# Kernel optimization log

Measured on AMD Instinct MI355X. Metric: run time of the kernel, lower is better.

The kernel has to match this reference:

```python
import jax, jax.numpy as jnp
import numpy as np

N_NODES = 50000
N_EDGES = 300000
IN_FEATS = 128
N_HIDDEN = 64
N_HEADS = 4
N_CLASSES = 47
NEG_SLOPE = 0.2


def setup_inputs() -> dict:
    key = jax.random.key(0)
    ks = jax.random.split(key, 16)
    s = 0.1
    inp = {
        "x": jax.random.normal(ks[0], (N_NODES, IN_FEATS), jnp.float32),
        "src": jax.random.randint(ks[1], (N_EDGES,), 0, N_NODES, jnp.int64 if jax.config.jax_enable_x64 else jnp.int32),
        "dst": jax.random.randint(ks[2], (N_EDGES,), 0, N_NODES, jnp.int64 if jax.config.jax_enable_x64 else jnp.int32),
        # layer 1: in_feats -> (heads, hidden)
        "W1": jax.random.normal(ks[3], (IN_FEATS, N_HEADS * N_HIDDEN), jnp.float32) * s,
        "al1": jax.random.normal(ks[4], (N_HEADS, N_HIDDEN), jnp.float32) * s,
        "ar1": jax.random.normal(ks[5], (N_HEADS, N_HIDDEN), jnp.float32) * s,
        "b1": jnp.zeros((N_HEADS * N_HIDDEN,), jnp.float32),
        # layer 2: heads*hidden -> (heads, hidden)
        "W2": jax.random.normal(ks[6], (N_HEADS * N_HIDDEN, N_HEADS * N_HIDDEN), jnp.float32) * s,
        "al2": jax.random.normal(ks[7], (N_HEADS, N_HIDDEN), jnp.float32) * s,
        "ar2": jax.random.normal(ks[8], (N_HEADS, N_HIDDEN), jnp.float32) * s,
        "b2": jnp.zeros((N_HEADS * N_HIDDEN,), jnp.float32),
        # layer 3: heads*hidden -> (1, n_classes)
        "W3": jax.random.normal(ks[9], (N_HEADS * N_HIDDEN, N_CLASSES), jnp.float32) * s,
        "al3": jax.random.normal(ks[10], (1, N_CLASSES), jnp.float32) * s,
        "ar3": jax.random.normal(ks[11], (1, N_CLASSES), jnp.float32) * s,
        "b3": jnp.zeros((N_CLASSES,), jnp.float32),
    }
    return inp


def gat_conv(h, src, dst, W, al, ar, b, n_nodes):
    """DGL GATConv (shared src/dst projection, edge-softmax over dst)."""
    H, D = al.shape
    feat = (h @ W).reshape(n_nodes, H, D)              # [N,H,D]
    el = jnp.sum(feat * al[None], axis=-1)             # [N,H]
    er = jnp.sum(feat * ar[None], axis=-1)             # [N,H]
    e = jax.nn.leaky_relu(el[src] + er[dst], NEG_SLOPE)  # [E,H]
    emax = jax.ops.segment_max(e, dst, num_segments=n_nodes)  # [N,H]
    emax = jnp.where(jnp.isfinite(emax), emax, 0.0)    # empty segments
    ee = jnp.exp(e - emax[dst])                        # [E,H]
    denom = jax.ops.segment_sum(ee, dst, num_segments=n_nodes)  # [N,H]
    alpha = ee / jnp.maximum(denom[dst], 1e-9)         # [E,H]
    msg = feat[src] * alpha[..., None]                 # [E,H,D]
    out = jax.ops.segment_sum(msg, dst, num_segments=n_nodes)   # [N,H,D]
    return out + b.reshape(1, H, D)


def reference(x, src, dst, W1, al1, ar1, b1, W2, al2, ar2, b2, W3, al3, ar3, b3):
    n = x.shape[0]
    h = gat_conv(x, src, dst, W1, al1, ar1, b1, n).reshape(n, -1)  # flatten heads
    h = gat_conv(h, src, dst, W2, al2, ar2, b2, n).reshape(n, -1)
    h = gat_conv(h, src, dst, W3, al3, ar3, b3, n)                 # [N,1,C]
    return h.mean(axis=1)                                          # [N,C]
```

## Files before the change

### kernel.cpp

```cpp
#include <hip/hip_runtime.h>
#include <cstddef>

#define GAT_N 50000
#define GAT_E 300000
#define SCAN_B 256

typedef short bf16x8 __attribute__((ext_vector_type(8)));
typedef float f32x4  __attribute__((ext_vector_type(4)));

__device__ __forceinline__ ushort f2bf(float f) {
    unsigned u = __float_as_uint(f);
    return (ushort)((u + 0x7fffu + ((u >> 16) & 1u)) >> 16);
}
__device__ __forceinline__ float bf2f(ushort h) {
    return __uint_as_float((unsigned)h << 16);
}


__global__ __launch_bounds__(256) void zero_ints(int* __restrict__ a, int n) {
    int i = blockIdx.x * blockDim.x + threadIdx.x;
    int stride = gridDim.x * blockDim.x;
    for (; i < n; i += stride) a[i] = 0;
}

__global__ __launch_bounds__(256) void count_k(
    const int* __restrict__ dst, int* __restrict__ cnt, int E)
{
    int e = blockIdx.x * blockDim.x + threadIdx.x;
    if (e < E) atomicAdd(&cnt[dst[e]], 1);
}

__global__ __launch_bounds__(256) void csr_partial(
    const int* __restrict__ cnt, int* __restrict__ partials, int N, int chunk)
{
    __shared__ int red[256];
    int b = blockIdx.x, t = threadIdx.x;
    int s = 0;
    for (int i = t; i < chunk; i += 256) {
        int idx = b * chunk + i;
        if (idx < N) s += cnt[idx];
    }
    red[t] = s;
    __syncthreads();
    for (int off = 128; off > 0; off >>= 1) {
        if (t < off) red[t] += red[t + off];
        __syncthreads();
    }
    if (t == 0) partials[b] = red[0];
}

__global__ __launch_bounds__(SCAN_B) void csr_scanp(
    int* __restrict__ partials, int* __restrict__ rowptr, int N)
{
    __shared__ int sc[SCAN_B];
    int t = threadIdx.x;
    int v = partials[t];
    sc[t] = v;
    __syncthreads();
    for (int off = 1; off < SCAN_B; off <<= 1) {
        int u = (t >= off) ? sc[t - off] : 0;
        __syncthreads();
        sc[t] += u;
        __syncthreads();
    }
    partials[t] = sc[t] - v;
    if (t == SCAN_B - 1) rowptr[N] = sc[t];
}

__global__ __launch_bounds__(256) void csr_write(
    const int* __restrict__ cnt, const int* __restrict__ partials,
    int* __restrict__ rowptr, int N, int chunk)
{
    __shared__ int sc[256];
    int b = blockIdx.x, t = threadIdx.x;
    int idx = b * chunk + t;
    int v = (t < chunk && idx < N) ? cnt[idx] : 0;
    sc[t] = v;
    __syncthreads();
    for (int off = 1; off < 256; off <<= 1) {
        int u = (t >= off) ? sc[t - off] : 0;
        __syncthreads();
        sc[t] += u;
        __syncthreads();
    }
    if (t < chunk && idx < N) rowptr[idx] = partials[b] + sc[t] - v;
}

__global__ __launch_bounds__(256) void scatter_k(
    const int* __restrict__ src, const int* __restrict__ dst,
    const int* __restrict__ rowptr, int* __restrict__ cursor,
    int* __restrict__ ssrc, int* __restrict__ sdst, int E)
{
    int e = blockIdx.x * blockDim.x + threadIdx.x;
    if (e >= E) return;
    int d = dst[e];
    int p = rowptr[d] + atomicAdd(&cursor[d], 1);
    ssrc[p] = src[e];
    sdst[p] = d;
}


__global__ __launch_bounds__(256) void convert_x(
    const float* __restrict__ x, ushort* __restrict__ Xh, ushort* __restrict__ Xl,
    long total4)
{
    long i = (long)blockIdx.x * blockDim.x + threadIdx.x;
    long stride = (long)gridDim.x * blockDim.x;
    for (; i < total4; i += stride) {
        float4 v = *(const float4*)(x + i * 4);
        ushort4 h, lo;
        h.x = f2bf(v.x); lo.x = f2bf(v.x - bf2f(h.x));
        h.y = f2bf(v.y); lo.y = f2bf(v.y - bf2f(h.y));
        h.z = f2bf(v.z); lo.z = f2bf(v.z - bf2f(h.z));
        h.w = f2bf(v.w); lo.w = f2bf(v.w - bf2f(h.w));
        *(ushort4*)(Xh + i * 4) = h;
        *(ushort4*)(Xl + i * 4) = lo;
    }
}

__global__ __launch_bounds__(256) void convert_w(
    const float* __restrict__ W, ushort* __restrict__ Wth, ushort* __restrict__ Wtl,
    int K, int M, int Mp)
{
    int idx = blockIdx.x * blockDim.x + threadIdx.x;
    if (idx >= Mp * K) return;
    int c = idx / K, k = idx - c * K;
    float v = (c < M) ? W[(size_t)k * M + c] : 0.f;
    ushort h = f2bf(v);
    Wth[idx] = h;
    Wtl[idx] = f2bf(v - bf2f(h));
}


#define LDK 40

__global__ __launch_bounds__(256) void gemm_feat(
    const ushort* __restrict__ Ah, const ushort* __restrict__ Al,
    const ushort* __restrict__ Wh, const ushort* __restrict__ Wl,
    const float* __restrict__ alw, const float* __restrict__ arw,
    float* __restrict__ feat, float* __restrict__ el, float* __restrict__ er,
    int N, int K, int M, int H, int D, int ldF)
{
    __shared__ ushort As_h[128 * LDK];
    __shared__ ushort As_l[128 * LDK];
    __shared__ ushort Bs_h[128 * LDK];
    __shared__ ushort Bs_l[128 * LDK];

    const int m0 = blockIdx.x * 128;
    const int n0 = blockIdx.y * 128;
    const int t = threadIdx.x;
    const int w = t >> 6, lane = t & 63;
    const int lr = lane & 15, lg = lane >> 4;
    const int wr = (w >> 1) * 64, wc = (w & 1) * 64;

    f32x4 acc[4][4] = {};

    for (int k0 = 0; k0 < K; k0 += 32) {
        #pragma unroll
        for (int l = 0; l < 2; ++l) {
            int idx = t + l * 256;
            int row = idx >> 2, kk = (idx & 3) * 8;
            bf16x8 vh = {}, vl = {};
            int gr = m0 + row;
            if (gr < N) {
                vh = *(const bf16x8*)(Ah + (size_t)gr * K + k0 + kk);
                vl = *(const bf16x8*)(Al + (size_t)gr * K + k0 + kk);
            }
            bf16x8 wh = *(const bf16x8*)(Wh + (size_t)(n0 + row) * K + k0 + kk);
            bf16x8 wl = *(const bf16x8*)(Wl + (size_t)(n0 + row) * K + k0 + kk);
            *(bf16x8*)&As_h[row * LDK + kk] = vh;
            *(bf16x8*)&As_l[row * LDK + kk] = vl;
            *(bf16x8*)&Bs_h[row * LDK + kk] = wh;
            *(bf16x8*)&Bs_l[row * LDK + kk] = wl;
        }
        __syncthreads();

        bf16x8 a_h[4], a_l[4];
        #pragma unroll
        for (int fi = 0; fi < 4; ++fi) {
            a_h[fi] = *(const bf16x8*)&As_h[(wr + fi * 16 + lr) * LDK + lg * 8];
            a_l[fi] = *(const bf16x8*)&As_l[(wr + fi * 16 + lr) * LDK + lg * 8];
        }
        #pragma unroll
        for (int fj = 0; fj < 4; ++fj) {
            bf16x8 b_h = *(const bf16x8*)&Bs_h[(wc + fj * 16 + lr) * LDK + lg * 8];
            bf16x8 b_l = *(const bf16x8*)&Bs_l[(wc + fj * 16 + lr) * LDK + lg * 8];
            #pragma unroll
            for (int fi = 0; fi < 4; ++fi) {
                acc[fi][fj] = __builtin_amdgcn_mfma_f32_16x16x32_bf16(a_h[fi], b_h, acc[fi][fj], 0, 0, 0);
                acc[fi][fj] = __builtin_amdgcn_mfma_f32_16x16x32_bf16(a_l[fi], b_h, acc[fi][fj], 0, 0, 0);
                acc[fi][fj] = __builtin_amdgcn_mfma_f32_16x16x32_bf16(a_h[fi], b_l, acc[fi][fj], 0, 0, 0);
            }
        }
        __syncthreads();
    }

    #pragma unroll
    for (int fi = 0; fi < 4; ++fi) {
        #pragma unroll
        for (int q = 0; q < 4; ++q) {
            int row = m0 + wr + fi * 16 + 4 * lg + q;
            if (row < N) {
                #pragma unroll
                for (int fj = 0; fj < 4; ++fj) {
                    int col = n0 + wc + fj * 16 + lr;
                    if (col < M) feat[(size_t)row * ldF + col] = acc[fi][fj][q];
                }
            }
        }
    }

    const int head = (n0 + wc) / D;
    if (head < H) {
        float alv[4], arv[4];
        #pragma unroll
        for (int fj = 0; fj < 4; ++fj) {
            int col = n0 + wc + fj * 16 + lr;
            alv[fj] = (col < M) ? alw[col] : 0.f;
            arv[fj] = (col < M) ? arw[col] : 0.f;
        }
        #pragma unroll
        for (int fi = 0; fi < 4; ++fi) {
            #pragma unroll
            for (int q = 0; q < 4; ++q) {
                float s1 = 0.f, s2 = 0.f;
                #pragma unroll
                for (int fj = 0; fj < 4; ++fj) {
                    s1 = fmaf(acc[fi][fj][q], alv[fj], s1);
                    s2 = fmaf(acc[fi][fj][q], arv[fj], s2);
                }
                #pragma unroll
                for (int mask = 1; mask <= 8; mask <<= 1) {
                    s1 += __shfl_xor(s1, mask);
                    s2 += __shfl_xor(s2, mask);
                }
                int row = m0 + wr + fi * 16 + 4 * lg + q;
                if (lr == 0 && row < N) {
                    el[(size_t)row * H + head] = s1;
                    er[(size_t)row * H + head] = s2;
                }
            }
        }
    }
}


__global__ __launch_bounds__(256) void edge_score4(
    const int* __restrict__ ssrc, const int* __restrict__ sdst,
    const float* __restrict__ el, const float* __restrict__ er,
    float* __restrict__ sc, int E)
{
    int p = blockIdx.x * blockDim.x + threadIdx.x;
    if (p >= E) return;
    int s = ssrc[p], d = sdst[p];
    float4 a = *(const float4*)(el + (size_t)s * 4);
    float4 b = *(const float4*)(er + (size_t)d * 4);
    float4 v;
    v.x = a.x + b.x; v.x = v.x > 0.f ? v.x : 0.2f * v.x;
    v.y = a.y + b.y; v.y = v.y > 0.f ? v.y : 0.2f * v.y;
    v.z = a.z + b.z; v.z = v.z > 0.f ? v.z : 0.2f * v.z;
    v.w = a.w + b.w; v.w = v.w > 0.f ? v.w : 0.2f * v.w;
    *(float4*)(sc + (size_t)p * 4) = v;
}

__global__ __launch_bounds__(256) void edge_score1(
    const int* __restrict__ ssrc, const int* __restrict__ sdst,
    const float* __restrict__ el, const float* __restrict__ er,
    float* __restrict__ sc, int E)
{
    int p = blockIdx.x * blockDim.x + threadIdx.x;
    if (p >= E) return;
    float v = el[ssrc[p]] + er[sdst[p]];
    sc[p] = v > 0.f ? v : 0.2f * v;
}


__global__ __launch_bounds__(256) void node_aggr256(
    const int* __restrict__ rowptr, const int* __restrict__ ssrc,
    const float* __restrict__ sc, const float* __restrict__ feat,
    const float* __restrict__ bias,
    ushort* __restrict__ Ah_out, ushort* __restrict__ Al_out, int N)
{
    int n = blockIdx.x * 4 + (threadIdx.x >> 6);
    if (n >= N) return;
    int lane = threadIdx.x & 63;
    int h = lane >> 4, sub = lane & 15;
    int beg = rowptr[n], end = rowptr[n + 1];

    float m = -__builtin_inff();
    for (int j = beg + sub; j < end; j += 16)
        m = fmaxf(m, sc[(size_t)j * 4 + h]);
    #pragma unroll
    for (int mask = 1; mask <= 8; mask <<= 1)
        m = fmaxf(m, __shfl_xor(m, mask));

    float denom = 0.f;
    for (int j = beg + sub; j < end; j += 16)
        denom += __expf(sc[(size_t)j * 4 + h] - m);
    #pragma unroll
    for (int mask = 1; mask <= 8; mask <<= 1)
        denom += __shfl_xor(denom, mask);

    float inv = 1.f / fmaxf(denom, 1e-9f);
    float ax = 0.f, ay = 0.f, az = 0.f, aw = 0.f;
    for (int j = beg; j < end; ++j) {
        float wgt = __expf(sc[(size_t)j * 4 + h] - m);
        int s = ssrc[j];
        float4 f = *(const float4*)(feat + (size_t)s * 256 + lane * 4);
        ax = fmaf(wgt, f.x, ax);
        ay = fmaf(wgt, f.y, ay);
        az = fmaf(wgt, f.z, az);
        aw = fmaf(wgt, f.w, aw);
    }
    float v0 = fmaf(ax, inv, bias[lane * 4 + 0]);
    float v1 = fmaf(ay, inv, bias[lane * 4 + 1]);
    float v2 = fmaf(az, inv, bias[lane * 4 + 2]);
    float v3 = fmaf(aw, inv, bias[lane * 4 + 3]);
    ushort4 hh, lo;
    hh.x = f2bf(v0); lo.x = f2bf(v0 - bf2f(hh.x));
    hh.y = f2bf(v1); lo.y = f2bf(v1 - bf2f(hh.y));
    hh.z = f2bf(v2); lo.z = f2bf(v2 - bf2f(hh.z));
    hh.w = f2bf(v3); lo.w = f2bf(v3 - bf2f(hh.w));
    *(ushort4*)(Ah_out + (size_t)n * 256 + lane * 4) = hh;
    *(ushort4*)(Al_out + (size_t)n * 256 + lane * 4) = lo;
}

__global__ __launch_bounds__(256) void node_aggr47(
    const int* __restrict__ rowptr, const int* __restrict__ ssrc,
    const float* __restrict__ sc, const float* __restrict__ feat,
    const float* __restrict__ bias, float* __restrict__ out, int N)
{
    int n = blockIdx.x * 4 + (threadIdx.x >> 6);
    if (n >= N) return;
    int lane = threadIdx.x & 63;
    int beg = rowptr[n], end = rowptr[n + 1];

    float m = -__builtin_inff();
    for (int j = beg + lane; j < end; j += 64)
        m = fmaxf(m, sc[j]);
    #pragma unroll
    for (int mask = 1; mask <= 32; mask <<= 1)
        m = fmaxf(m, __shfl_xor(m, mask));

    float denom = 0.f;
    for (int j = beg + lane; j < end; j += 64)
        denom += __expf(sc[j] - m);
    #pragma unroll
    for (int mask = 1; mask <= 32; mask <<= 1)
        denom += __shfl_xor(denom, mask);

    float inv = 1.f / fmaxf(denom, 1e-9f);
    float acc = 0.f;
    for (int j = beg; j < end; ++j) {
        float wgt = __expf(sc[j] - m);
        int s = ssrc[j];
        float f = (lane < 47) ? feat[(size_t)s * 48 + lane] : 0.f;
        acc = fmaf(wgt, f, acc);
    }
    if (lane < 47)
        out[(size_t)n * 47 + lane] = fmaf(acc, inv, bias[lane]);
}


extern "C" void kernel_launch(void* const* d_in, const int* in_sizes, int n_in,
                              void* d_out, int out_size, void* d_ws, size_t ws_size,
                              hipStream_t stream) {
    const float* x   = (const float*)d_in[0];
    const int*   src = (const int*)d_in[1];
    const int*   dst = (const int*)d_in[2];
    const float* W1  = (const float*)d_in[3];
    const float* al1 = (const float*)d_in[4];
    const float* ar1 = (const float*)d_in[5];
    const float* b1  = (const float*)d_in[6];
    const float* W2  = (const float*)d_in[7];
    const float* al2 = (const float*)d_in[8];
    const float* ar2 = (const float*)d_in[9];
    const float* b2  = (const float*)d_in[10];
    const float* W3  = (const float*)d_in[11];
    const float* al3 = (const float*)d_in[12];
    const float* ar3 = (const float*)d_in[13];
    const float* b3  = (const float*)d_in[14];
    float* out = (float*)d_out;

    const int N = GAT_N, E = GAT_E;
    const int chunk = (N + SCAN_B - 1) / SCAN_B;

    char* wsb = (char*)d_ws;
    size_t o = 0;
    float*  feat  = (float*)(wsb + o);  o += (size_t)N * 256 * 4;
    ushort* Ah    = (ushort*)(wsb + o); o += (size_t)N * 256 * 2;
    ushort* Al    = (ushort*)(wsb + o); o += (size_t)N * 256 * 2;
    float*  el    = (float*)(wsb + o);  o += (size_t)N * 4 * 4;
    float*  er    = (float*)(wsb + o);  o += (size_t)N * 4 * 4;
    int* rowptr   = (int*)(wsb + o);    o += (size_t)(N + 1) * 4;
    int* cnt      = (int*)(wsb + o);    o += (size_t)N * 4;
    int* cursor   = (int*)(wsb + o);    o += (size_t)N * 4;
    int* ssrc     = (int*)(wsb + o);    o += (size_t)E * 4;
    int* sdst     = (int*)(wsb + o);    o += (size_t)E * 4;
    float* scbuf  = (float*)(wsb + o);  o += (size_t)E * 4 * 4;
    int* partials = (int*)(wsb + o);    o += (size_t)SCAN_B * 4;
    ushort* Wt1h  = (ushort*)(wsb + o); o += (size_t)256 * 128 * 2;
    ushort* Wt1l  = (ushort*)(wsb + o); o += (size_t)256 * 128 * 2;
    ushort* Wt2h  = (ushort*)(wsb + o); o += (size_t)256 * 256 * 2;
    ushort* Wt2l  = (ushort*)(wsb + o); o += (size_t)256 * 256 * 2;
    ushort* Wt3h  = (ushort*)(wsb + o); o += (size_t)128 * 256 * 2;
    ushort* Wt3l  = (ushort*)(wsb + o); o += (size_t)128 * 256 * 2;
    ushort* Xh = Ah;
    ushort* Xl = Al;

    dim3 blk(256);
    int gE = (E + 255) / 256;
    int gN = (N + 3) / 4;
    dim3 gemmG((N + 127) / 128, 2);
    dim3 gemmG3((N + 127) / 128, 1);

    zero_ints<<<64, blk, 0, stream>>>(cnt, 2 * N);
    count_k<<<gE, blk, 0, stream>>>(dst, cnt, E);
    csr_partial<<<SCAN_B, blk, 0, stream>>>(cnt, partials, N, chunk);
    csr_scanp<<<1, SCAN_B, 0, stream>>>(partials, rowptr, N);
    csr_write<<<SCAN_B, blk, 0, stream>>>(cnt, partials, rowptr, N, chunk);
    scatter_k<<<gE, blk, 0, stream>>>(src, dst, rowptr, cursor, ssrc, sdst, E);

    convert_x<<<2048, blk, 0, stream>>>(x, Xh, Xl, (long)N * 128 / 4);
    convert_w<<<(256 * 128 + 255) / 256, blk, 0, stream>>>(W1, Wt1h, Wt1l, 128, 256, 256);
    convert_w<<<(256 * 256 + 255) / 256, blk, 0, stream>>>(W2, Wt2h, Wt2l, 256, 256, 256);
    convert_w<<<(128 * 256 + 255) / 256, blk, 0, stream>>>(W3, Wt3h, Wt3l, 256, 47, 128);

    gemm_feat<<<gemmG, blk, 0, stream>>>(Xh, Xl, Wt1h, Wt1l, al1, ar1,
                                         feat, el, er, N, 128, 256, 4, 64, 256);
    edge_score4<<<gE, blk, 0, stream>>>(ssrc, sdst, el, er, scbuf, E);
    node_aggr256<<<gN, blk, 0, stream>>>(rowptr, ssrc, scbuf, feat, b1, Ah, Al, N);

    gemm_feat<<<gemmG, blk, 0, stream>>>(Ah, Al, Wt2h, Wt2l, al2, ar2,
                                         feat, el, er, N, 256, 256, 4, 64, 256);
    edge_score4<<<gE, blk, 0, stream>>>(ssrc, sdst, el, er, scbuf, E);
    node_aggr256<<<gN, blk, 0, stream>>>(rowptr, ssrc, scbuf, feat, b2, Ah, Al, N);

    gemm_feat<<<gemmG3, blk, 0, stream>>>(Ah, Al, Wt3h, Wt3l, al3, ar3,
                                          feat, el, er, N, 256, 47, 1, 47, 48);
    edge_score1<<<gE, blk, 0, stream>>>(ssrc, sdst, el, er, scbuf, E);
    node_aggr47<<<gN, blk, 0, stream>>>(rowptr, ssrc, scbuf, feat, b3, out, N);
}
```

Measured before the change: 332.2 us.

## Halve GEMM row tile to 64 and unroll edge gather loops by four

The feature GEMM now uses a 64-row tile instead of 128, doubling the grid and halving accumulator registers per thread, to raise occupancy and spread 50k rows across more blocks. Separately, the aggregation kernels for the 256-wide and 47-class layers unroll the per-edge gather loop by four so several independent feature loads are in flight at once. The smaller tile cuts reuse of the W tile, so each block reloads B more often relative to its useful work.

```diff
diff --git a/kernel.cpp b/kernel.cpp
--- a/kernel.cpp
+++ b/kernel.cpp
@@ -141,43 +141,44 @@
     float* __restrict__ feat, float* __restrict__ el, float* __restrict__ er,
     int N, int K, int M, int H, int D, int ldF)
 {
-    __shared__ ushort As_h[128 * LDK];
-    __shared__ ushort As_l[128 * LDK];
+    __shared__ ushort As_h[64 * LDK];
+    __shared__ ushort As_l[64 * LDK];
     __shared__ ushort Bs_h[128 * LDK];
     __shared__ ushort Bs_l[128 * LDK];
 
-    const int m0 = blockIdx.x * 128;
+    const int m0 = blockIdx.x * 64;
     const int n0 = blockIdx.y * 128;
     const int t = threadIdx.x;
     const int w = t >> 6, lane = t & 63;
     const int lr = lane & 15, lg = lane >> 4;
-    const int wr = (w >> 1) * 64, wc = (w & 1) * 64;
-
-    f32x4 acc[4][4] = {};
+    const int wr = (w >> 1) * 32, wc = (w & 1) * 64;
+
+    f32x4 acc[2][4] = {};
 
     for (int k0 = 0; k0 < K; k0 += 32) {
-        #pragma unroll
-        for (int l = 0; l < 2; ++l) {
-            int idx = t + l * 256;
-            int row = idx >> 2, kk = (idx & 3) * 8;
+        {
+            int row = t >> 2, kk = (t & 3) * 8;
             bf16x8 vh = {}, vl = {};
             int gr = m0 + row;
             if (gr < N) {
                 vh = *(const bf16x8*)(Ah + (size_t)gr * K + k0 + kk);
                 vl = *(const bf16x8*)(Al + (size_t)gr * K + k0 + kk);
             }
-            bf16x8 wh = *(const bf16x8*)(Wh + (size_t)(n0 + row) * K + k0 + kk);
-            bf16x8 wl = *(const bf16x8*)(Wl + (size_t)(n0 + row) * K + k0 + kk);
             *(bf16x8*)&As_h[row * LDK + kk] = vh;
             *(bf16x8*)&As_l[row * LDK + kk] = vl;
-            *(bf16x8*)&Bs_h[row * LDK + kk] = wh;
-            *(bf16x8*)&Bs_l[row * LDK + kk] = wl;
-        }
-        __syncthreads();
-
-        bf16x8 a_h[4], a_l[4];
-        #pragma unroll
-        for (int fi = 0; fi < 4; ++fi) {
+        }
+        #pragma unroll
+        for (int l = 0; l < 2; ++l) {
+            int idx = t + l * 256;
+            int row = idx >> 2, kk = (idx & 3) * 8;
+            *(bf16x8*)&Bs_h[row * LDK + kk] = *(const bf16x8*)(Wh + (size_t)(n0 + row) * K + k0 + kk);
+            *(bf16x8*)&Bs_l[row * LDK + kk] = *(const bf16x8*)(Wl + (size_t)(n0 + row) * K + k0 + kk);
+        }
+        __syncthreads();
+
+        bf16x8 a_h[2], a_l[2];
+        #pragma unroll
+        for (int fi = 0; fi < 2; ++fi) {
             a_h[fi] = *(const bf16x8*)&As_h[(wr + fi * 16 + lr) * LDK + lg * 8];
             a_l[fi] = *(const bf16x8*)&As_l[(wr + fi * 16 + lr) * LDK + lg * 8];
         }
@@ -186,7 +187,7 @@
             bf16x8 b_h = *(const bf16x8*)&Bs_h[(wc + fj * 16 + lr) * LDK + lg * 8];
             bf16x8 b_l = *(const bf16x8*)&Bs_l[(wc + fj * 16 + lr) * LDK + lg * 8];
             #pragma unroll
-            for (int fi = 0; fi < 4; ++fi) {
+            for (int fi = 0; fi < 2; ++fi) {
                 acc[fi][fj] = __builtin_amdgcn_mfma_f32_16x16x32_bf16(a_h[fi], b_h, acc[fi][fj], 0, 0, 0);
                 acc[fi][fj] = __builtin_amdgcn_mfma_f32_16x16x32_bf16(a_l[fi], b_h, acc[fi][fj], 0, 0, 0);
                 acc[fi][fj] = __builtin_amdgcn_mfma_f32_16x16x32_bf16(a_h[fi], b_l, acc[fi][fj], 0, 0, 0);
@@ -196,7 +197,7 @@
     }
 
     #pragma unroll
-    for (int fi = 0; fi < 4; ++fi) {
+    for (int fi = 0; fi < 2; ++fi) {
         #pragma unroll
         for (int q = 0; q < 4; ++q) {
             int row = m0 + wr + fi * 16 + 4 * lg + q;
@@ -220,7 +221,7 @@
             arv[fj] = (col < M) ? arw[col] : 0.f;
         }
         #pragma unroll
-        for (int fi = 0; fi < 4; ++fi) {
+        for (int fi = 0; fi < 2; ++fi) {
             #pragma unroll
             for (int q = 0; q < 4; ++q) {
                 float s1 = 0.f, s2 = 0.f;
@@ -303,7 +304,23 @@
 
     float inv = 1.f / fmaxf(denom, 1e-9f);
     float ax = 0.f, ay = 0.f, az = 0.f, aw = 0.f;
-    for (int j = beg; j < end; ++j) {
+    int j = beg;
+    for (; j + 4 <= end; j += 4) {
+        int s0 = ssrc[j + 0], s1 = ssrc[j + 1], s2 = ssrc[j + 2], s3 = ssrc[j + 3];
+        float w0 = __expf(sc[(size_t)(j + 0) * 4 + h] - m);
+        float w1 = __expf(sc[(size_t)(j + 1) * 4 + h] - m);
+        float w2 = __expf(sc[(size_t)(j + 2) * 4 + h] - m);
+        float w3 = __expf(sc[(size_t)(j + 3) * 4 + h] - m);
+        float4 f0 = *(const float4*)(feat + (size_t)s0 * 256 + lane * 4);
+        float4 f1 = *(const float4*)(feat + (size_t)s1 * 256 + lane * 4);
+        float4 f2 = *(const float4*)(feat + (size_t)s2 * 256 + lane * 4);
+        float4 f3 = *(const float4*)(feat + (size_t)s3 * 256 + lane * 4);
+        ax = fmaf(w0, f0.x, fmaf(w1, f1.x, fmaf(w2, f2.x, fmaf(w3, f3.x, ax))));
+        ay = fmaf(w0, f0.y, fmaf(w1, f1.y, fmaf(w2, f2.y, fmaf(w3, f3.y, ay))));
+        az = fmaf(w0, f0.z, fmaf(w1, f1.z, fmaf(w2, f2.z, fmaf(w3, f3.z, az))));
+        aw = fmaf(w0, f0.w, fmaf(w1, f1.w, fmaf(w2, f2.w, fmaf(w3, f3.w, aw))));
+    }
+    for (; j < end; ++j) {
         float wgt = __expf(sc[(size_t)j * 4 + h] - m);
         int s = ssrc[j];
         float4 f = *(const float4*)(feat + (size_t)s * 256 + lane * 4);
@@ -351,7 +368,20 @@
 
     float inv = 1.f / fmaxf(denom, 1e-9f);
     float acc = 0.f;
-    for (int j = beg; j < end; ++j) {
+    int j = beg;
+    for (; j + 4 <= end; j += 4) {
+        int s0 = ssrc[j + 0], s1 = ssrc[j + 1], s2 = ssrc[j + 2], s3 = ssrc[j + 3];
+        float w0 = __expf(sc[j + 0] - m);
+        float w1 = __expf(sc[j + 1] - m);
+        float w2 = __expf(sc[j + 2] - m);
+        float w3 = __expf(sc[j + 3] - m);
+        float f0 = (lane < 47) ? feat[(size_t)s0 * 48 + lane] : 0.f;
+        float f1 = (lane < 47) ? feat[(size_t)s1 * 48 + lane] : 0.f;
+        float f2 = (lane < 47) ? feat[(size_t)s2 * 48 + lane] : 0.f;
+        float f3 = (lane < 47) ? feat[(size_t)s3 * 48 + lane] : 0.f;
+        acc = fmaf(w0, f0, fmaf(w1, f1, fmaf(w2, f2, fmaf(w3, f3, acc))));
+    }
+    for (; j < end; ++j) {
         float wgt = __expf(sc[j] - m);
         int s = ssrc[j];
         float f = (lane < 47) ? feat[(size_t)s * 48 + lane] : 0.f;
@@ -411,8 +441,8 @@
     dim3 blk(256);
     int gE = (E + 255) / 256;
     int gN = (N + 3) / 4;
-    dim3 gemmG((N + 127) / 128, 2);
-    dim3 gemmG3((N + 127) / 128, 1);
+    dim3 gemmG((N + 63) / 64, 2);
+    dim3 gemmG3((N + 63) / 64, 1);
 
     zero_ints<<<64, blk, 0, stream>>>(cnt, 2 * N);
     count_k<<<gE, blk, 0, stream>>>(dst, cnt, E);
```

New measurement: 311.5 us. 6.2% less time.
